# Performance work log

Measured on AMD Instinct MI355X. Metric: run time of the kernel, lower is better.

## Reference

```python
import jax, jax.numpy as jnp
import numpy as np

N_QUBITS = 8
N_LAYERS = 2
DIM = 2 ** N_QUBITS  # 256

# ---- 2x2 gate matrices (PennyLane conventions) ----

def _rx(t):
    # RX(t) = [[cos(t/2), -i sin(t/2)], [-i sin(t/2), cos(t/2)]]
    c = jnp.cos(t / 2).astype(jnp.complex64)
    s = (-1j * jnp.sin(t / 2)).astype(jnp.complex64)
    return jnp.stack([jnp.stack([c, s], -1), jnp.stack([s, c], -1)], -2)

def _ry(t):
    c = jnp.cos(t / 2).astype(jnp.complex64)
    s = jnp.sin(t / 2).astype(jnp.complex64)
    return jnp.stack([jnp.stack([c, -s], -1), jnp.stack([s, c], -1)], -2)

def _rz(t):
    e = jnp.exp(-1j * (t / 2).astype(jnp.complex64))
    z = jnp.zeros_like(e)
    return jnp.stack([jnp.stack([e, z], -1), jnp.stack([z, jnp.conj(e)], -1)], -2)

# ---- batched state-vector gate application ----
# state layout: (B, 2, 2, ..., 2); wire 0 is the most-significant axis (PennyLane default.qubit)

def _apply_1q(state, gate, wire):
    ax = 1 + wire
    state = jnp.moveaxis(state, ax, -1)
    if gate.ndim == 2:  # shared gate (trainable weights)
        state = jnp.einsum('...i,ji->...j', state, gate)
    else:               # per-sample gate (angle embedding), gate: (B,2,2)
        state = jnp.einsum('b...i,bji->b...j', state, gate)
    return jnp.moveaxis(state, -1, ax)

def _apply_cnot(state, ctrl, tgt):
    a, b = 1 + ctrl, 1 + tgt
    state = jnp.moveaxis(state, (a, b), (-2, -1))
    # flip target amplitudes where control bit = 1
    state = jnp.concatenate([state[..., 0:1, :], state[..., 1:2, ::-1]], axis=-2)
    return jnp.moveaxis(state, (-2, -1), (a, b))


def _signs():
    idx = np.arange(DIM)
    # bit of wire i in basis index (wire 0 = MSB)
    s = np.stack([1.0 - 2.0 * ((idx >> (N_QUBITS - 1 - i)) & 1)
                  for i in range(N_QUBITS)], axis=1)
    return jnp.asarray(s.astype(np.float32))  # (DIM, N_QUBITS)


def setup_inputs() -> dict:
    key = jax.random.key(0)
    k1, k2 = jax.random.split(key)
    B = 131072
    x = jax.random.normal(k1, (B, N_QUBITS), dtype=jnp.float32)
    weights = jax.random.uniform(k2, (N_LAYERS, N_QUBITS, 3), dtype=jnp.float32,
                                 minval=0.0, maxval=2.0 * np.pi)
    return {"x": x, "weights": weights}


def reference(x, weights):
    B = x.shape[0]
    state = jnp.zeros((B, DIM), jnp.complex64).at[:, 0].set(1.0)
    state = state.reshape((B,) + (2,) * N_QUBITS)
    # AngleEmbedding: RX(x[:, q]) on each wire (default rotation='X')
    for q in range(N_QUBITS):
        state = _apply_1q(state, _rx(x[:, q]), q)
    for l in range(N_LAYERS):
        for q in range(N_QUBITS):
            state = _apply_1q(state, _rx(weights[l, q, 0]), q)
            state = _apply_1q(state, _ry(weights[l, q, 1]), q)
            state = _apply_1q(state, _rz(weights[l, q, 2]), q)
        for q in range(N_QUBITS):
            state = _apply_cnot(state, q, (q + 1) % N_QUBITS)
    probs = jnp.abs(state.reshape(B, DIM)) ** 2  # (B, 256)
    return (probs @ _signs()).astype(jnp.float32)  # <Z_i> per wire, (B, 8)
```

## Files before the change

kernel.cpp:

```cpp
#include <hip/hip_runtime.h>
#include <math.h>


typedef float f2 __attribute__((ext_vector_type(2)));
typedef float f4 __attribute__((ext_vector_type(4)));
typedef _Float16 half8 __attribute__((ext_vector_type(8)));

__device__ __forceinline__ f2 cmul_pk(f2 a, f2 b) {
    f2 t, d;
    asm("v_pk_mul_f32 %0, %1, %2 op_sel:[0,0] op_sel_hi:[0,1]"
        : "=v"(t) : "v"(a), "v"(b));
    asm("v_pk_fma_f32 %0, %1, %2, %3 op_sel:[1,1,0] op_sel_hi:[1,0,1] neg_lo:[1,0,0] neg_hi:[0,0,0]"
        : "=v"(d) : "v"(a), "v"(b), "v"(t));
    return d;
}
__device__ __forceinline__ unsigned cmulh(unsigned a, unsigned b) {
    unsigned t, d;
    asm("v_pk_mul_f16 %0, %1, %2 op_sel:[0,0] op_sel_hi:[0,1]"
        : "=v"(t) : "v"(a), "v"(b));
    asm("v_pk_fma_f16 %0, %1, %2, %3 op_sel:[1,1,0] op_sel_hi:[1,0,1] neg_lo:[1,0,0] neg_hi:[0,0,0]"
        : "=v"(d) : "v"(a), "v"(b), "v"(t));
    return d;
}
__device__ __forceinline__ unsigned pkh(f2 v) {
    auto pk = __builtin_amdgcn_cvt_pkrtz(v.x, v.y);
    unsigned u; __builtin_memcpy(&u, &pk, 4);
    return u;
}

__global__ void qnn_setup(const float* __restrict__ w, float* __restrict__ p) {
    int t = threadIdx.x;
    if (t < 8) {
        int q = t;
        float cb = cosf(w[q*3+1]*0.5f), sb = sinf(w[q*3+1]*0.5f);
        float cg = cosf(w[q*3+2]*0.5f), sg = sinf(w[q*3+2]*0.5f);
        p[q] = w[q*3+0];
        float* K = p + 8 + q*8;
        K[0] = cg*cb;  K[1] = -sg*cb;
        K[2] = sg*sb;  K[3] = cg*sb;
        K[4] = cg*sb;  K[5] = sg*sb;
        K[6] = sg*cb;  K[7] = -cg*cb;
    }
    float G[8][2][2][2];
    for (int q = 0; q < 8; ++q) {
        const float* wq = w + (8+q)*3;
        float ca = cosf(wq[0]*0.5f), sa = sinf(wq[0]*0.5f);
        float cb = cosf(wq[1]*0.5f), sb = sinf(wq[1]*0.5f);
        float cg = cosf(wq[2]*0.5f), sg = sinf(wq[2]*0.5f);
        float A = cb*ca, Bv = sb*sa, C = sb*ca, D = cb*sa;
        float g00r = cg*A + sg*Bv, g00i = cg*Bv - sg*A;
        float g01r = -(cg*C + sg*D), g01i = sg*C - cg*D;
        G[q][0][0][0]=g00r;  G[q][0][0][1]=g00i;
        G[q][0][1][0]=g01r;  G[q][0][1][1]=g01i;
        G[q][1][0][0]=-g01r; G[q][1][0][1]=g01i;
        G[q][1][1][0]=g00r;  G[q][1][1][1]=-g00i;
    }
    int m = t & 15, k2 = t >> 4;
    float ar = 1.f, ai = 0.f, br = 1.f, bi = 0.f;
    for (int j = 0; j < 4; ++j) {
        int bm = (m >> (3-j)) & 1, bk = (k2 >> (3-j)) & 1;
        float gr = G[j][bm][bk][0],  gi = G[j][bm][bk][1];
        float nr = ar*gr - ai*gi, ni = ar*gi + ai*gr; ar = nr; ai = ni;
        float hr = G[4+j][bm][bk][0], hi = G[4+j][bm][bk][1];
        float mr = br*hr - bi*hi, mi = br*hi + bi*hr; br = mr; bi = mi;
    }
    _Float16* A1 = (_Float16*)((char*)p + 512);
    _Float16* A2 = A1 + 512;
    _Float16* B1 = A1 + 1024;
    _Float16* B2 = A1 + 1536;
    int p0 = ((k2 >> 3)*16 + m)*8 + (k2 & 7);
    int k3 = k2 + 16;
    int p1 = ((k3 >> 3)*16 + m)*8 + (k3 & 7);
    A1[p0] = (_Float16)ar;   A1[p1] = (_Float16)(-ai);
    A2[p0] = (_Float16)ai;   A2[p1] = (_Float16)ar;
    B1[p0] = (_Float16)br;   B1[p1] = (_Float16)(-bi);
    B2[p0] = (_Float16)bi;   B2[p1] = (_Float16)br;

    const int cls[8] = {2, 0, 1, 2, 2, 2, 2, 2};
    const int msk[8] = {31, 48, 48, 48, 56, 60, 62, 63};
    _Float16* SG = (_Float16*)((char*)p + 4608);
    for (int e = t; e < 512; e += 256) {
        int tt = e >> 6, l = e & 63, n = l & 15, quad = l >> 4;
        for (int j = 0; j < 8; ++j) {
            int k  = tt*32 + quad*8 + j;
            int Lp = k >> 2, c = k & 3;
            float v = 0.f;
            if (n < 8 && c == cls[n])
                v = (__popc(msk[n] & Lp) & 1) ? -1.f : 1.f;
            SG[e*8 + j] = (_Float16)v;
        }
    }
}

#define WAVE_LDS 8192

__global__ __launch_bounds__(256, 5) void qnn_main(
        const float* __restrict__ x, const float* __restrict__ p,
        float* __restrict__ out, int B)
{
    __shared__ __align__(16) char smem[4 * WAVE_LDS];
    const int lane = threadIdx.x & 63;
    const int wid  = threadIdx.x >> 6;
    const int L = lane;
    const int b0 = (blockIdx.x * 4 + wid) * 16;
    if (b0 >= B) return;

    char* wb  = smem + wid * WAVE_LDS;
    char* Sb  = wb;
    char* Mb  = wb + 1280;
    char* THb = wb + 2560;
    char* CFb = wb + 3072;
    char* V4t = wb + 4160;
    char* RFb = wb + 4416;
    char* Rb  = wb + 5440;
    f4*   VT  = (f4*)Rb;

    const half8* fr = (const half8*)((const char*)p + 512);
    half8 A1f = fr[L], A2f = fr[64 + L], B1f = fr[128 + L], B2f = fr[192 + L];
    const half8* sgt = (const half8*)((const char*)p + 4608);

    {
        int sI = L >> 2, qp = (L & 3) * 2;
        float2 xv  = ((const float2*)x)[(size_t)(b0 + sI)*4 + (L & 3)];
        float2 w0p = ((const float2*)p)[qp >> 1];
        const f4* Kt = (const f4*)(p + 8);
#pragma unroll
        for (int u = 0; u < 2; ++u) {
            int q = qp + u;
            float ang = (u ? xv.y : xv.x) + (u ? w0p.y : w0p.x);
            float rev = ang * 0.07957747154594767f;
            float ca = __builtin_amdgcn_cosf(rev);
            float sa = __builtin_amdgcn_sinf(rev);
            f4 Ka = Kt[q*2], Kb = Kt[q*2+1];
            f4 v;
            v.x = ca*Ka.x + sa*Ka.z;  v.y = ca*Ka.y + sa*Ka.w;
            v.z = ca*Kb.x + sa*Kb.z;  v.w = ca*Kb.y + sa*Kb.w;
            VT[sI*8 + q] = v;
        }
    }

    {
        int sI = L >> 2, j = L & 3;
        const f4* Vs = VT + sI*8;
        f4 q0v = Vs[0], q1v = Vs[1], q2v = Vs[2], q3v = Vs[3];
        f4 q4v = Vs[4], q5v = Vs[5], q6v = Vs[6], q7v = Vs[7];
        f2 V0a = {q0v.x,q0v.y}, V0b = {q0v.z,q0v.w};
        f2 V1a = {q1v.x,q1v.y}, V1b = {q1v.z,q1v.w};
        f2 V2a = {q2v.x,q2v.y}, V2b = {q2v.z,q2v.w};
        f2 V3a = {q3v.x,q3v.y}, V3b = {q3v.z,q3v.w};
        f2 V4a = {q4v.x,q4v.y}, V4bv = {q4v.z,q4v.w};
        f2 V5a = {q5v.x,q5v.y}, V5b = {q5v.z,q5v.w};
        f2 V6a = {q6v.x,q6v.y}, V6b = {q6v.z,q6v.w};
        f2 V7a = {q7v.x,q7v.y}, V7b = {q7v.z,q7v.w};
        int t1 = j >> 1, t2 = j & 1;
        f2 th0 = cmul_pk(t1 ? V0b : V0a, t2 ? V1b : V1a);
        f2 th1 = cmul_pk(t1 ? V0a : V0b, t2 ? V1a : V1b);
        *(uint2*)(THb + sI*32 + j*8) = (uint2){pkh(th0), pkh(th1)};
        int col3 = j >> 1, col2 = j & 1;
        f2 v5s  = (col3 ^ col2) ? V5b : V5a;
        f2 p6_0 = cmul_pk(v5s, col2 ? V6b : V6a);
        f2 p6_1 = cmul_pk(v5s, col2 ? V6a : V6b);
#pragma unroll
        for (int c = 0; c < 4; ++c) {
            int c1 = c >> 1, c0 = c & 1;
            f2 cf = cmul_pk(c1 ? p6_1 : p6_0, (c1 ^ c0) ? V7b : V7a);
            *(unsigned*)(CFb + sI*68 + (4*j + c)*4) = pkh(cf);
        }
        if (j < 2) {
            f2 lo = j ? V4bv : V4a, hi = j ? V4a : V4bv;
            *(uint2*)(V4t + sI*16 + j*8) = (uint2){pkh(lo), pkh(hi)};
        }
        unsigned rr[4];
#pragma unroll
        for (int r = 0; r < 4; ++r) {
            int r1 = r >> 1, r0 = r & 1;
            f2 rf = cmul_pk(((j & 1) ^ r1) ? V2b : V2a, (r1 ^ r0) ? V3b : V3a);
            rr[r] = pkh(rf);
        }
        *(uint4*)(RFb + sI*64 + j*16) = (uint4){rr[0], rr[1], rr[2], rr[3]};
    }

    const int hq  = L >> 4;
    const int col = L & 15;
    const int th_t1 = hq >> 1, th_t2 = (hq >> 1) ^ (hq & 1);
    char* THl = THb + ((th_t1*2 + th_t2)*2 + (col & 1))*4;
    char* CFl = CFb + col*4;
    char* V4l = V4t + (col >> 3)*8;
    char* RFl = RFb + hq*16;

    char* wS  = Sb + col*80 + hq*16;
    char* rS  = Sb + col*80 + (hq & 1)*32 + (hq >> 1)*8;
    char* wM  = Mb + hq*320 + col*4;
    char* rM  = Mb + col*80 + (hq & 1)*32;
    char* Rw  = Rb + L*8;
    char* Rr  = Rb + (col & 3)*544 + hq*16;
    const unsigned selM = (hq >> 1) ? 0x07060302u : 0x05040100u;
    const f4 zz = {0.f, 0.f, 0.f, 0.f};

    for (int h = 0; h < 4; ++h) {
        for (int s4 = 0; s4 < 4; ++s4) {
            const int s = h*4 + s4;
            unsigned u  = *(const unsigned*)(THl + s*32);
            unsigned cf = *(const unsigned*)(CFl + s*68);
            uint2   v4  = *(const uint2*)(V4l + s*16);
            uint4   rf  = *(const uint4*)(RFl + s*64);
            unsigned g  = cmulh(u, cf);
            unsigned gl = cmulh(g, v4.x);
            unsigned gh = cmulh(g, v4.y);
            unsigned a0 = cmulh(rf.x, gl);
            unsigned a1 = cmulh(rf.y, gh);
            unsigned a2 = cmulh(rf.z, gl);
            unsigned a3 = cmulh(rf.w, gh);
            uint2 pr = { __builtin_amdgcn_perm(a1, a0, 0x05040100u),
                         __builtin_amdgcn_perm(a3, a2, 0x05040100u) };
            uint2 pi = { __builtin_amdgcn_perm(a1, a0, 0x07060302u),
                         __builtin_amdgcn_perm(a3, a2, 0x07060302u) };
            *(uint4*)wS = (uint4){pr.x, pr.y, pi.x, pi.y};
            uint2 lo = *(uint2*)rS;
            uint2 hi = *(uint2*)(rS + 16);
            uint4 sv = {lo.x, lo.y, hi.x, hi.y};
            half8 sfrag;
            __builtin_memcpy(&sfrag, &sv, 16);
            f4 mr = __builtin_amdgcn_mfma_f32_16x16x32_f16(A1f, sfrag, zz, 0, 0, 0);
            f4 mi = __builtin_amdgcn_mfma_f32_16x16x32_f16(A2f, sfrag, zz, 0, 0, 0);
            *(unsigned*)(wM +   0) = pkh((f2){mr[0], mi[0]});
            *(unsigned*)(wM +  80) = pkh((f2){mr[1], mi[1]});
            *(unsigned*)(wM + 160) = pkh((f2){mr[2], mi[2]});
            *(unsigned*)(wM + 240) = pkh((f2){mr[3], mi[3]});
            uint4 da = *(uint4*)rM;
            uint4 db = *(uint4*)(rM + 16);
            uint4 nf;
            nf.x = __builtin_amdgcn_perm(da.y, da.x, selM);
            nf.y = __builtin_amdgcn_perm(da.w, da.z, selM);
            nf.z = __builtin_amdgcn_perm(db.y, db.x, selM);
            nf.w = __builtin_amdgcn_perm(db.w, db.z, selM);
            half8 nfrag;
            __builtin_memcpy(&nfrag, &nf, 16);
            f4 pr4 = __builtin_amdgcn_mfma_f32_16x16x32_f16(nfrag, B1f, zz, 0, 0, 0);
            f4 pi4 = __builtin_amdgcn_mfma_f32_16x16x32_f16(nfrag, B2f, zz, 0, 0, 0);
            float Q0 = pr4[0]*pr4[0] + pi4[0]*pi4[0];
            float Q1 = pr4[1]*pr4[1] + pi4[1]*pi4[1];
            float Q2 = pr4[2]*pr4[2] + pi4[2]*pi4[2];
            float Q3 = pr4[3]*pr4[3] + pi4[3]*pi4[3];
            float s01 = Q0 + Q1, s23 = Q2 + Q3;
            float S00 = s01 + s23;
            float S10 = s01 - s23;
            float S11 = (Q0 - Q1) - (Q2 - Q3);
            uint2 wv = { pkh((f2){S00, S10}), pkh((f2){S11, 0.f}) };
            *(uint2*)(Rw + s4*544) = wv;
        }
        f4 acc = zz;
#pragma unroll
        for (int tt = 0; tt < 8; ++tt) {
            uint4 rv = *(uint4*)(Rr + tt*64);
            half8 af;
            __builtin_memcpy(&af, &rv, 16);
            acc = __builtin_amdgcn_mfma_f32_16x16x32_f16(af, sgt[tt*64 + L], acc, 0, 0, 0);
        }
        if (hq == 0 && col < 8) {
            size_t base = (size_t)(b0 + h*4) * 8 + col;
            out[base     ] = acc[0];
            out[base +  8] = acc[1];
            out[base + 16] = acc[2];
            out[base + 24] = acc[3];
        }
    }
}

extern "C" void kernel_launch(void* const* d_in, const int* in_sizes, int n_in,
                              void* d_out, int out_size, void* d_ws, size_t ws_size,
                              hipStream_t stream) {
    const float* x = (const float*)d_in[0];
    const float* w = (const float*)d_in[1];
    float* outp    = (float*)d_out;
    float* params  = (float*)d_ws;
    int B = in_sizes[0] / 8;

    qnn_setup<<<1, 256, 0, stream>>>(w, params);
    int blocks = (B + 63) / 64;
    qnn_main<<<blocks, 256, 0, stream>>>(x, params, outp, B);
}
```

Baseline: 87.91 us.

## Chain 16x16x16 MFMAs in registers to drop LDS staging between stages

Replaces the two 16x16x32 complex MFMA stages with pairs of 16x16x16 MFMAs whose operand layouts let the first stage's output feed the second directly from registers. This removes the LDS write/read round trips and byte permutes for the S and M buffers. Per-wave LDS shrinks, so launch bounds rise to allow more resident waves. The cost is eight smaller MFMAs instead of four larger ones, a reorganised qubit-to-axis mapping with new sign tables, and fp16 rounding of the intermediate.

```diff
diff --git a/kernel.cpp b/kernel.cpp
--- a/kernel.cpp
+++ b/kernel.cpp
@@ -4,6 +4,7 @@
 
 typedef float f2 __attribute__((ext_vector_type(2)));
 typedef float f4 __attribute__((ext_vector_type(4)));
+typedef _Float16 half4 __attribute__((ext_vector_type(4)));
 typedef _Float16 half8 __attribute__((ext_vector_type(8)));
 
 __device__ __forceinline__ f2 cmul_pk(f2 a, f2 b) {
@@ -26,6 +27,13 @@
     auto pk = __builtin_amdgcn_cvt_pkrtz(v.x, v.y);
     unsigned u; __builtin_memcpy(&u, &pk, 4);
     return u;
+}
+__device__ __forceinline__ half4 h4(uint2 u) {
+    half4 h; __builtin_memcpy(&h, &u, 8);
+    return h;
+}
+__device__ __forceinline__ f4 mfma16(half4 a, half4 b, f4 c) {
+    return __builtin_amdgcn_mfma_f32_16x16x16f16(a, b, c, 0, 0, 0);
 }
 
 __global__ void qnn_setup(const float* __restrict__ w, float* __restrict__ p) {
@@ -64,20 +72,22 @@
         float hr = G[4+j][bm][bk][0], hi = G[4+j][bm][bk][1];
         float mr = br*hr - bi*hi, mi = br*hi + bi*hr; br = mr; bi = mi;
     }
-    _Float16* A1 = (_Float16*)((char*)p + 512);
-    _Float16* A2 = A1 + 512;
-    _Float16* B1 = A1 + 1024;
-    _Float16* B2 = A1 + 1536;
-    int p0 = ((k2 >> 3)*16 + m)*8 + (k2 & 7);
-    int k3 = k2 + 16;
-    int p1 = ((k3 >> 3)*16 + m)*8 + (k3 & 7);
-    A1[p0] = (_Float16)ar;   A1[p1] = (_Float16)(-ai);
-    A2[p0] = (_Float16)ai;   A2[p1] = (_Float16)ar;
-    B1[p0] = (_Float16)br;   B1[p1] = (_Float16)(-bi);
-    B2[p0] = (_Float16)bi;   B2[p1] = (_Float16)br;
-
-    const int cls[8] = {2, 0, 1, 2, 2, 2, 2, 2};
-    const int msk[8] = {31, 48, 48, 48, 56, 60, 62, 63};
+    _Float16* S1Ar  = (_Float16*)((char*)p +  512);
+    _Float16* S1Ai  = (_Float16*)((char*)p + 1024);
+    _Float16* S1nAi = (_Float16*)((char*)p + 1536);
+    _Float16* S2Br  = (_Float16*)((char*)p + 2048);
+    _Float16* S2Bi  = (_Float16*)((char*)p + 2560);
+    _Float16* S2nBi = (_Float16*)((char*)p + 3072);
+    int idx = ((k2 >> 2)*16 + m)*4 + (k2 & 3);
+    S1Ar[idx]  = (_Float16)ar;
+    S1Ai[idx]  = (_Float16)ai;
+    S1nAi[idx] = (_Float16)(-ai);
+    S2Br[idx]  = (_Float16)br;
+    S2Bi[idx]  = (_Float16)bi;
+    S2nBi[idx] = (_Float16)(-bi);
+
+    const int cls[8] = {2, 0, 0, 0, 0, 0, 1, 2};
+    const int msk[8] = {55, 12, 14, 15, 47, 63, 63, 63};
     _Float16* SG = (_Float16*)((char*)p + 4608);
     for (int e = t; e < 512; e += 256) {
         int tt = e >> 6, l = e & 63, n = l & 15, quad = l >> 4;
@@ -92,9 +102,9 @@
     }
 }
 
-#define WAVE_LDS 8192
-
-__global__ __launch_bounds__(256, 5) void qnn_main(
+#define WAVE_LDS 5120
+
+__global__ __launch_bounds__(256, 6) void qnn_main(
         const float* __restrict__ x, const float* __restrict__ p,
         float* __restrict__ out, int B)
 {
@@ -106,17 +116,20 @@
     if (b0 >= B) return;
 
     char* wb  = smem + wid * WAVE_LDS;
-    char* Sb  = wb;
-    char* Mb  = wb + 1280;
-    char* THb = wb + 2560;
-    char* CFb = wb + 3072;
-    char* V4t = wb + 4160;
-    char* RFb = wb + 4416;
-    char* Rb  = wb + 5440;
+    char* THb = wb;
+    char* CFb = wb + 512;
+    char* V4t = wb + 1600;
+    char* RFb = wb + 1856;
+    char* Rb  = wb + 2880;
     f4*   VT  = (f4*)Rb;
 
-    const half8* fr = (const half8*)((const char*)p + 512);
-    half8 A1f = fr[L], A2f = fr[64 + L], B1f = fr[128 + L], B2f = fr[192 + L];
+    const uint2* ft = (const uint2*)((const char*)p + 512);
+    half4 Art  = h4(ft[      L]);
+    half4 Ait  = h4(ft[ 64 + L]);
+    half4 nAit = h4(ft[128 + L]);
+    half4 Brf  = h4(ft[192 + L]);
+    half4 Bif  = h4(ft[256 + L]);
+    half4 nBif = h4(ft[320 + L]);
     const half8* sgt = (const half8*)((const char*)p + 4608);
 
     {
@@ -187,14 +200,8 @@
     char* CFl = CFb + col*4;
     char* V4l = V4t + (col >> 3)*8;
     char* RFl = RFb + hq*16;
-
-    char* wS  = Sb + col*80 + hq*16;
-    char* rS  = Sb + col*80 + (hq & 1)*32 + (hq >> 1)*8;
-    char* wM  = Mb + hq*320 + col*4;
-    char* rM  = Mb + col*80 + (hq & 1)*32;
     char* Rw  = Rb + L*8;
     char* Rr  = Rb + (col & 3)*544 + hq*16;
-    const unsigned selM = (hq >> 1) ? 0x07060302u : 0x05040100u;
     const f4 zz = {0.f, 0.f, 0.f, 0.f};
 
     for (int h = 0; h < 4; ++h) {
@@ -211,37 +218,22 @@
             unsigned a1 = cmulh(rf.y, gh);
             unsigned a2 = cmulh(rf.z, gl);
             unsigned a3 = cmulh(rf.w, gh);
-            uint2 pr = { __builtin_amdgcn_perm(a1, a0, 0x05040100u),
-                         __builtin_amdgcn_perm(a3, a2, 0x05040100u) };
-            uint2 pi = { __builtin_amdgcn_perm(a1, a0, 0x07060302u),
-                         __builtin_amdgcn_perm(a3, a2, 0x07060302u) };
-            *(uint4*)wS = (uint4){pr.x, pr.y, pi.x, pi.y};
-            uint2 lo = *(uint2*)rS;
-            uint2 hi = *(uint2*)(rS + 16);
-            uint4 sv = {lo.x, lo.y, hi.x, hi.y};
-            half8 sfrag;
-            __builtin_memcpy(&sfrag, &sv, 16);
-            f4 mr = __builtin_amdgcn_mfma_f32_16x16x32_f16(A1f, sfrag, zz, 0, 0, 0);
-            f4 mi = __builtin_amdgcn_mfma_f32_16x16x32_f16(A2f, sfrag, zz, 0, 0, 0);
-            *(unsigned*)(wM +   0) = pkh((f2){mr[0], mi[0]});
-            *(unsigned*)(wM +  80) = pkh((f2){mr[1], mi[1]});
-            *(unsigned*)(wM + 160) = pkh((f2){mr[2], mi[2]});
-            *(unsigned*)(wM + 240) = pkh((f2){mr[3], mi[3]});
-            uint4 da = *(uint4*)rM;
-            uint4 db = *(uint4*)(rM + 16);
-            uint4 nf;
-            nf.x = __builtin_amdgcn_perm(da.y, da.x, selM);
-            nf.y = __builtin_amdgcn_perm(da.w, da.z, selM);
-            nf.z = __builtin_amdgcn_perm(db.y, db.x, selM);
-            nf.w = __builtin_amdgcn_perm(db.w, db.z, selM);
-            half8 nfrag;
-            __builtin_memcpy(&nfrag, &nf, 16);
-            f4 pr4 = __builtin_amdgcn_mfma_f32_16x16x32_f16(nfrag, B1f, zz, 0, 0, 0);
-            f4 pi4 = __builtin_amdgcn_mfma_f32_16x16x32_f16(nfrag, B2f, zz, 0, 0, 0);
-            float Q0 = pr4[0]*pr4[0] + pi4[0]*pi4[0];
-            float Q1 = pr4[1]*pr4[1] + pi4[1]*pi4[1];
-            float Q2 = pr4[2]*pr4[2] + pi4[2]*pi4[2];
-            float Q3 = pr4[3]*pr4[3] + pi4[3]*pi4[3];
+            half4 Srf = h4((uint2){ __builtin_amdgcn_perm(a1, a0, 0x05040100u),
+                                    __builtin_amdgcn_perm(a3, a2, 0x05040100u) });
+            half4 Sif = h4((uint2){ __builtin_amdgcn_perm(a1, a0, 0x07060302u),
+                                    __builtin_amdgcn_perm(a3, a2, 0x07060302u) });
+            f4 Tr4 = mfma16(Sif, nAit, mfma16(Srf, Art, zz));
+            f4 Ti4 = mfma16(Sif, Art,  mfma16(Srf, Ait, zz));
+            half4 Trf = h4((uint2){ pkh((f2){Tr4[0], Tr4[1]}),
+                                    pkh((f2){Tr4[2], Tr4[3]}) });
+            half4 Tif = h4((uint2){ pkh((f2){Ti4[0], Ti4[1]}),
+                                    pkh((f2){Ti4[2], Ti4[3]}) });
+            f4 Pr4 = mfma16(nBif, Tif, mfma16(Brf, Trf, zz));
+            f4 Pi4 = mfma16(Bif,  Trf, mfma16(Brf, Tif, zz));
+            float Q0 = Pr4[0]*Pr4[0] + Pi4[0]*Pi4[0];
+            float Q1 = Pr4[1]*Pr4[1] + Pi4[1]*Pi4[1];
+            float Q2 = Pr4[2]*Pr4[2] + Pi4[2]*Pi4[2];
+            float Q3 = Pr4[3]*Pr4[3] + Pi4[3]*Pi4[3];
             float s01 = Q0 + Q1, s23 = Q2 + Q3;
             float S00 = s01 + s23;
             float S10 = s01 - s23;
```

Result: faster. 83.89 us (-4.6%).
